# Kernel optimization log

Hardware: AMD Instinct MI355X
Metric: run time of the kernel (lower is better)

## Reference

```python
import jax, jax.numpy as jnp
import numpy as np

B, N, C = 4, 2048, 768
H = 12
HD = C // H
SCALE = HD ** -0.5


def setup_inputs() -> dict:
    key = jax.random.key(0)
    k1, k2, k3 = jax.random.split(key, 3)
    x = jax.random.normal(k1, (B, N, C), dtype=jnp.float32)
    w_qkv = jax.random.normal(k2, (3 * C, C), dtype=jnp.float32) * (C ** -0.5)
    w_proj = jax.random.normal(k3, (C, C), dtype=jnp.float32) * (C ** -0.5)
    b_proj = jnp.zeros((C,), dtype=jnp.float32)
    return {"x": x, "w_qkv": w_qkv, "w_proj": w_proj, "b_proj": b_proj}


def reference(x, w_qkv, w_proj, b_proj):
    Bx, Nx, Cx = x.shape
    # qkv linear: x @ W^T -> [B, N, 3C], then split into heads
    qkv = jnp.einsum('bnc,dc->bnd', x, w_qkv)
    qkv = qkv.reshape(Bx, Nx, 3, H, HD).transpose(2, 0, 3, 1, 4)  # [3, B, H, N, HD]
    q, k, v = qkv[0], qkv[1], qkv[2]
    attn = jnp.einsum('bhqd,bhkd->bhqk', q, k) * SCALE  # [B, H, N, N]
    attn = jax.nn.softmax(attn, axis=-1)
    out = jnp.einsum('bhqk,bhkd->bhqd', attn, v)  # [B, H, N, HD]
    out = out.transpose(0, 2, 1, 3).reshape(Bx, Nx, Cx)
    out = jnp.einsum('bnc,dc->bnd', out, w_proj) + b_proj
    return out
```

## Files before the change

kernel.cpp:

```cpp
#include <hip/hip_runtime.h>
#include <hip/hip_bf16.h>
#include <stdint.h>

#define DI __device__ __forceinline__

typedef __bf16 bf16x8 __attribute__((ext_vector_type(8)));
typedef float f32x4 __attribute__((ext_vector_type(4)));
typedef uint32_t u32x4 __attribute__((ext_vector_type(4)));
typedef unsigned short u16;

DI u16 f2bf(float f) {
  union { float f; uint32_t u; } x; x.f = f;
  uint32_t r = (x.u + 0x7FFFu + ((x.u >> 16) & 1u)) >> 16;
  return (u16)r;
}
DI bf16x8 load16(const u16* p) { return *(const bf16x8*)p; }

DI void async_copy16(void* lds, const void* g) {
  __builtin_amdgcn_global_load_lds(
      (const __attribute__((address_space(1))) uint32_t*)g,
      (__attribute__((address_space(3))) uint32_t*)lds, 16, 0, 0);
}

DI f32x4 mfma16(bf16x8 a, bf16x8 b, f32x4 c) {
  return __builtin_amdgcn_mfma_f32_16x16x32_bf16(a, b, c, 0, 0, 0);
}

DI uint32_t pk_bf16(float a, float b) {
  union { __hip_bfloat162 v; uint32_t u; } r;
  r.v = __float22bfloat162_rn(make_float2(a, b));
  return r.u;
}

DI void permlane32_swap(uint32_t &a, uint32_t &b) {
  asm("v_permlane32_swap_b32 %0, %1" : "+v"(a), "+v"(b));
}

#define QSCALE (0.125f * 1.44269504088896340736f)

__global__ __launch_bounds__(256)
void cvt_all(const float* __restrict__ s0, u16* __restrict__ d0, int n0,
             const float* __restrict__ s1, u16* __restrict__ d1, int n1,
             const float* __restrict__ s2, u16* __restrict__ d2, int n2) {
  int i = (blockIdx.x * 256 + threadIdx.x) * 4;
  const float* s; u16* d;
  if (i < n0) { s = s0 + i; d = d0 + i; }
  else if (i < n0 + n1) { s = s1 + (i - n0); d = d1 + (i - n0); }
  else if (i < n0 + n1 + n2) { s = s2 + (i - n0 - n1); d = d2 + (i - n0 - n1); }
  else return;
  float4 v = *(const float4*)s;
  ushort4 o;
  o.x = f2bf(v.x); o.y = f2bf(v.y); o.z = f2bf(v.z); o.w = f2bf(v.w);
  *(ushort4*)d = o;
}

__global__ __launch_bounds__(256)
void gemm_qkv(const u16* __restrict__ A, const u16* __restrict__ Bm,
              u16* __restrict__ Qb, u16* __restrict__ Kb, u16* __restrict__ Vt,
              int M, int N, int K) {
  __shared__ u16 As[128 * 32];
  __shared__ u16 Bs[128 * 32];

  const int tid  = threadIdx.x;
  const int lane = tid & 63;
  const int wave = tid >> 6;
  const int lb  = blockIdx.x + 18 * blockIdx.y;
  const int swz = (lb & 7) * 144 + (lb >> 3);
  const int n0 = (swz % 18) * 128;
  const int m0 = (swz / 18) * 128;
  const int wm = (wave & 1) * 64;
  const int wn = (wave >> 1) * 64;
  const int c = lane & 15;
  const int g = lane >> 4;

  f32x4 acc[4][4] = {};

  for (int k0 = 0; k0 < K; k0 += 32) {
#pragma unroll
    for (int i = 0; i < 2; ++i) {
      int j = i * 256 + tid;
      int row = j >> 2;
      int col = (j & 3) * 8;
      async_copy16(&As[j * 8], &A[(size_t)(m0 + row) * K + k0 + col]);
      async_copy16(&Bs[j * 8], &Bm[(size_t)(n0 + row) * K + k0 + col]);
    }
    __syncthreads();

    bf16x8 af[4], bfr[4];
#pragma unroll
    for (int t = 0; t < 4; ++t) {
      af[t]  = *(const bf16x8*)&As[(wm + t * 16 + c) * 32 + g * 8];
      bfr[t] = *(const bf16x8*)&Bs[(wn + t * 16 + c) * 32 + g * 8];
    }
#pragma unroll
    for (int mt = 0; mt < 4; ++mt)
#pragma unroll
      for (int nt = 0; nt < 4; ++nt)
        acc[mt][nt] = mfma16(af[mt], bfr[nt], acc[mt][nt]);
    __syncthreads();
  }

  if (n0 < 768) {
#pragma unroll
    for (int nt = 0; nt < 4; ++nt) {
      int col = n0 + wn + nt * 16 + c;
#pragma unroll
      for (int mt = 0; mt < 4; ++mt)
#pragma unroll
        for (int r = 0; r < 4; ++r) {
          int row = m0 + wm + mt * 16 + g * 4 + r;
          Qb[(size_t)row * 768 + col] = f2bf(acc[mt][nt][r] * QSCALE);
        }
    }
  } else if (n0 < 1536) {
#pragma unroll
    for (int nt = 0; nt < 4; ++nt) {
      int col = n0 - 768 + wn + nt * 16 + c;
#pragma unroll
      for (int mt = 0; mt < 4; ++mt)
#pragma unroll
        for (int r = 0; r < 4; ++r) {
          int row = m0 + wm + mt * 16 + g * 4 + r;
          Kb[(size_t)row * 768 + col] = f2bf(acc[mt][nt][r]);
        }
    }
  } else {
#pragma unroll
    for (int nt = 0; nt < 4; ++nt) {
      int cv = n0 - 1536 + wn + nt * 16 + c;
      int hv = cv >> 6, d = cv & 63;
#pragma unroll
      for (int mt = 0; mt < 4; ++mt) {
        int row = m0 + wm + mt * 16 + g * 4;
        int b = row >> 11, nn = row & 2047;
        ushort4 o;
        o.x = f2bf(acc[mt][nt][0]); o.y = f2bf(acc[mt][nt][1]);
        o.z = f2bf(acc[mt][nt][2]); o.w = f2bf(acc[mt][nt][3]);
        *(ushort4*)&Vt[(((size_t)b * 12 + hv) * 64 + d) * 2048 + nn] = o;
      }
    }
  }
}

__global__ __launch_bounds__(256)
void gemm_proj(const u16* __restrict__ A, const u16* __restrict__ Bm,
               const float* __restrict__ bias, float* __restrict__ Co,
               int M, int N, int K) {
  __shared__ u16 As[128 * 32];
  __shared__ u16 Bs[128 * 32];

  const int tid  = threadIdx.x;
  const int lane = tid & 63;
  const int wave = tid >> 6;
  const int lb  = blockIdx.x + 6 * blockIdx.y;
  const int swz = (lb & 7) * 48 + (lb >> 3);
  const int n0 = (swz % 6) * 128;
  const int m0 = (swz / 6) * 128;
  const int wm = (wave & 1) * 64;
  const int wn = (wave >> 1) * 64;
  const int c = lane & 15;
  const int g = lane >> 4;

  f32x4 acc[4][4] = {};

  for (int k0 = 0; k0 < K; k0 += 32) {
#pragma unroll
    for (int i = 0; i < 2; ++i) {
      int j = i * 256 + tid;
      int row = j >> 2;
      int col = (j & 3) * 8;
      async_copy16(&As[j * 8], &A[(size_t)(m0 + row) * K + k0 + col]);
      async_copy16(&Bs[j * 8], &Bm[(size_t)(n0 + row) * K + k0 + col]);
    }
    __syncthreads();

    bf16x8 af[4], bfr[4];
#pragma unroll
    for (int t = 0; t < 4; ++t) {
      af[t]  = *(const bf16x8*)&As[(wm + t * 16 + c) * 32 + g * 8];
      bfr[t] = *(const bf16x8*)&Bs[(wn + t * 16 + c) * 32 + g * 8];
    }
#pragma unroll
    for (int mt = 0; mt < 4; ++mt)
#pragma unroll
      for (int nt = 0; nt < 4; ++nt)
        acc[mt][nt] = mfma16(af[mt], bfr[nt], acc[mt][nt]);
    __syncthreads();
  }

#pragma unroll
  for (int nt = 0; nt < 4; ++nt) {
    int col = n0 + wn + nt * 16 + c;
    float bv = bias[col];
#pragma unroll
    for (int mt = 0; mt < 4; ++mt)
#pragma unroll
      for (int r = 0; r < 4; ++r) {
        int row = m0 + wm + mt * 16 + g * 4 + r;
        Co[(size_t)row * N + col] = acc[mt][nt][r] + bv;
      }
  }
}

__global__ __launch_bounds__(256)
void attn_flash(const u16* __restrict__ Qb, const u16* __restrict__ Kb,
                const u16* __restrict__ Vt, u16* __restrict__ out) {
  __shared__ u16 Ks[2][2 * 64 * 32];
  __shared__ u16 Vs[2][2 * 64 * 32];

  const int tid  = threadIdx.x;
  const int lane = tid & 63;
  const int wave = tid >> 6;
  const int bid = blockIdx.x;
  const int swz = (bid & 7) * 96 + (bid >> 3);
  const int qchunk = swz & 15;
  const int h = (swz >> 4) % 12;
  const int b = swz / 192;
  const int q0 = qchunk * 128 + wave * 32;
  const int c = lane & 15;
  const int g = lane >> 4;
  const int g_odd = g & 1;

  const u16* Qp = Qb + (size_t)b * 2048 * 768 + h * 64;
  const u16* Kp = Kb + (size_t)b * 2048 * 768 + h * 64;
  const u16* Vp = Vt + ((size_t)b * 12 + h) * 64 * 2048;

  const bf16x8 qf0 = load16(&Qp[(size_t)(q0 + c) * 768 + g * 8]);
  const bf16x8 qf1 = load16(&Qp[(size_t)(q0 + c) * 768 + 32 + g * 8]);
  const bf16x8 qg0 = load16(&Qp[(size_t)(q0 + 16 + c) * 768 + g * 8]);
  const bf16x8 qg1 = load16(&Qp[(size_t)(q0 + 16 + c) * 768 + 32 + g * 8]);

  const int kk = tid >> 2;
  const int ch = (tid & 3) * 8;

  float lsum0 = 0.f, lsum1 = 0.f;
  f32x4 o0[4] = {}, o1[4] = {};

  async_copy16(&Ks[0][tid * 8],        &Kp[(size_t)kk * 768 + ch]);
  async_copy16(&Ks[0][2048 + tid * 8], &Kp[(size_t)kk * 768 + 32 + ch]);
  async_copy16(&Vs[0][tid * 8],        &Vp[(size_t)kk * 2048 + ch]);
  async_copy16(&Vs[0][2048 + tid * 8], &Vp[(size_t)kk * 2048 + 32 + ch]);

  int cur = 0;
  for (int k0 = 0; k0 < 2048; k0 += 64) {
    __syncthreads();

    if (k0 + 64 < 2048) {
      int nxt = cur ^ 1, kn = k0 + 64;
      async_copy16(&Ks[nxt][tid * 8],        &Kp[(size_t)(kn + kk) * 768 + ch]);
      async_copy16(&Ks[nxt][2048 + tid * 8], &Kp[(size_t)(kn + kk) * 768 + 32 + ch]);
      async_copy16(&Vs[nxt][tid * 8],        &Vp[(size_t)kk * 2048 + kn + ch]);
      async_copy16(&Vs[nxt][2048 + tid * 8], &Vp[(size_t)kk * 2048 + kn + 32 + ch]);
    }

    f32x4 s0[4] = {}, s1[4] = {};
#pragma unroll
    for (int kt = 0; kt < 4; ++kt) {
      bf16x8 kf0 = *(const bf16x8*)&Ks[cur][(kt * 16 + c) * 32 + g * 8];
      bf16x8 kf1 = *(const bf16x8*)&Ks[cur][2048 + (kt * 16 + c) * 32 + g * 8];
      s0[kt] = mfma16(kf0, qf0, s0[kt]);
      s0[kt] = mfma16(kf1, qf1, s0[kt]);
      s1[kt] = mfma16(kf0, qg0, s1[kt]);
      s1[kt] = mfma16(kf1, qg1, s1[kt]);
    }

    bf16x8 PA0[2], PA1[2];
#pragma unroll
    for (int kt2 = 0; kt2 < 2; ++kt2) {
#pragma unroll
      for (int sub = 0; sub < 2; ++sub) {
        const f32x4 sa = sub ? s1[2 * kt2] : s0[2 * kt2];
        const f32x4 sb = sub ? s1[2 * kt2 + 1] : s0[2 * kt2 + 1];
        float e0 = __builtin_amdgcn_exp2f(sa[0]);
        float e1 = __builtin_amdgcn_exp2f(sa[1]);
        float e2 = __builtin_amdgcn_exp2f(sa[2]);
        float e3 = __builtin_amdgcn_exp2f(sa[3]);
        float f0 = __builtin_amdgcn_exp2f(sb[0]);
        float f1 = __builtin_amdgcn_exp2f(sb[1]);
        float f2 = __builtin_amdgcn_exp2f(sb[2]);
        float f3 = __builtin_amdgcn_exp2f(sb[3]);
        float sum = ((e0 + e1) + (e2 + e3)) + ((f0 + f1) + (f2 + f3));
        if (sub) lsum1 += sum; else lsum0 += sum;
        uint32_t E0 = pk_bf16(e0, e1);
        uint32_t E1 = pk_bf16(e2, e3);
        uint32_t F0 = pk_bf16(f0, f1);
        uint32_t F1 = pk_bf16(f2, f3);
        permlane32_swap(E0, F0);
        permlane32_swap(E1, F1);
        uint32_t Z0 = __shfl_xor(F0, 16);
        uint32_t Z1 = __shfl_xor(F1, 16);
        uint32_t Y0 = __shfl_xor(E0, 16);
        uint32_t Y1 = __shfl_xor(E1, 16);
        union { u32x4 u; bf16x8 v; } pa;
        pa.u.x = g_odd ? Z0 : E0;
        pa.u.y = g_odd ? Z1 : E1;
        pa.u.z = g_odd ? F0 : Y0;
        pa.u.w = g_odd ? F1 : Y1;
        if (sub) PA1[kt2] = pa.v; else PA0[kt2] = pa.v;
      }
    }

#pragma unroll
    for (int kt2 = 0; kt2 < 2; ++kt2) {
#pragma unroll
      for (int dt = 0; dt < 4; ++dt) {
        bf16x8 vf = *(const bf16x8*)&Vs[cur][kt2 * 2048 + (dt * 16 + c) * 32 + g * 8];
        o0[dt] = mfma16(PA0[kt2], vf, o0[dt]);
        o1[dt] = mfma16(PA1[kt2], vf, o1[dt]);
      }
    }
    cur ^= 1;
  }

  float t0 = lsum0 + __shfl_xor(lsum0, 16);
  t0 += __shfl_xor(t0, 32);
  float t1 = lsum1 + __shfl_xor(lsum1, 16);
  t1 += __shfl_xor(t1, 32);
  float inv0 = 1.f / t0;
  float inv1 = 1.f / t1;
  float invr0[4], invr1[4];
#pragma unroll
  for (int r = 0; r < 4; ++r) {
    invr0[r] = __shfl(inv0, g * 4 + r);
    invr1[r] = __shfl(inv1, g * 4 + r);
  }

#pragma unroll
  for (int dt = 0; dt < 4; ++dt)
#pragma unroll
    for (int r = 0; r < 4; ++r) {
      int n = q0 + g * 4 + r;
      out[(size_t)(b * 2048 + n) * 768 + h * 64 + dt * 16 + c] =
          f2bf(o0[dt][r] * invr0[r]);
      out[(size_t)(b * 2048 + n + 16) * 768 + h * 64 + dt * 16 + c] =
          f2bf(o1[dt][r] * invr1[r]);
    }
}

extern "C" void kernel_launch(void* const* d_in, const int* in_sizes, int n_in,
                              void* d_out, int out_size, void* d_ws, size_t ws_size,
                              hipStream_t stream) {
  const float* x      = (const float*)d_in[0];
  const float* w_qkv  = (const float*)d_in[1];
  const float* w_proj = (const float*)d_in[2];
  const float* b_proj = (const float*)d_in[3];
  float* out = (float*)d_out;

  const int M = 8192;
  const int C = 768;
  const int NQKV = 2304;

  u16* xb     = (u16*)d_ws;
  u16* wqkvb  = xb + (size_t)M * C;
  u16* wprojb = wqkvb + (size_t)NQKV * C;
  u16* Qb     = wprojb + (size_t)C * C;
  u16* Kb     = Qb + (size_t)M * C;
  u16* Vt     = Kb + (size_t)M * C;
  u16* attn   = Vt + (size_t)M * C;

  dim3 blk(256);
  const int n0 = M * C, n1 = NQKV * C, n2 = C * C;
  cvt_all<<<dim3((n0 + n1 + n2) / 1024), blk, 0, stream>>>(
      x, xb, n0, w_qkv, wqkvb, n1, w_proj, wprojb, n2);

  gemm_qkv<<<dim3(NQKV / 128, M / 128), blk, 0, stream>>>(
      xb, wqkvb, Qb, Kb, Vt, M, NQKV, C);
  attn_flash<<<dim3(4 * 12 * 16), blk, 0, stream>>>(Qb, Kb, Vt, attn);
  gemm_proj<<<dim3(C / 128, M / 128), blk, 0, stream>>>(
      attn, wprojb, b_proj, out, M, C, C);
}
```

Before: 229.5 us.

## Stage K/V through registers with XOR-swizzled LDS layout in flash attention

```diff
diff --git a/kernel.cpp b/kernel.cpp
--- a/kernel.cpp
+++ b/kernel.cpp
@@ -220,6 +220,7 @@
   const int c = lane & 15;
   const int g = lane >> 4;
   const int g_odd = g & 1;
+  const int sw = (g ^ (c & 3)) * 8;
 
   const u16* Qp = Qb + (size_t)b * 2048 * 768 + h * 64;
   const u16* Kp = Kb + (size_t)b * 2048 * 768 + h * 64;
@@ -230,34 +231,39 @@
   const bf16x8 qg0 = load16(&Qp[(size_t)(q0 + 16 + c) * 768 + g * 8]);
   const bf16x8 qg1 = load16(&Qp[(size_t)(q0 + 16 + c) * 768 + 32 + g * 8]);
 
-  const int kk = tid >> 2;
-  const int ch = (tid & 3) * 8;
+  const int kk  = tid >> 2;
+  const int chs = (((tid >> 2) & 3) ^ (tid & 3)) * 8;
 
   float lsum0 = 0.f, lsum1 = 0.f;
   f32x4 o0[4] = {}, o1[4] = {};
 
-  async_copy16(&Ks[0][tid * 8],        &Kp[(size_t)kk * 768 + ch]);
-  async_copy16(&Ks[0][2048 + tid * 8], &Kp[(size_t)kk * 768 + 32 + ch]);
-  async_copy16(&Vs[0][tid * 8],        &Vp[(size_t)kk * 2048 + ch]);
-  async_copy16(&Vs[0][2048 + tid * 8], &Vp[(size_t)kk * 2048 + 32 + ch]);
+  uint4 rk0 = *(const uint4*)&Kp[(size_t)kk * 768 + chs];
+  uint4 rk1 = *(const uint4*)&Kp[(size_t)kk * 768 + 32 + chs];
+  uint4 rv0 = *(const uint4*)&Vp[(size_t)kk * 2048 + chs];
+  uint4 rv1 = *(const uint4*)&Vp[(size_t)kk * 2048 + 32 + chs];
+  *(uint4*)&Ks[0][tid * 8]        = rk0;
+  *(uint4*)&Ks[0][2048 + tid * 8] = rk1;
+  *(uint4*)&Vs[0][tid * 8]        = rv0;
+  *(uint4*)&Vs[0][2048 + tid * 8] = rv1;
 
   int cur = 0;
   for (int k0 = 0; k0 < 2048; k0 += 64) {
     __syncthreads();
 
-    if (k0 + 64 < 2048) {
-      int nxt = cur ^ 1, kn = k0 + 64;
-      async_copy16(&Ks[nxt][tid * 8],        &Kp[(size_t)(kn + kk) * 768 + ch]);
-      async_copy16(&Ks[nxt][2048 + tid * 8], &Kp[(size_t)(kn + kk) * 768 + 32 + ch]);
-      async_copy16(&Vs[nxt][tid * 8],        &Vp[(size_t)kk * 2048 + kn + ch]);
-      async_copy16(&Vs[nxt][2048 + tid * 8], &Vp[(size_t)kk * 2048 + kn + 32 + ch]);
+    const bool pf = (k0 + 64 < 2048);
+    if (pf) {
+      int kn = k0 + 64;
+      rk0 = *(const uint4*)&Kp[(size_t)(kn + kk) * 768 + chs];
+      rk1 = *(const uint4*)&Kp[(size_t)(kn + kk) * 768 + 32 + chs];
+      rv0 = *(const uint4*)&Vp[(size_t)kk * 2048 + kn + chs];
+      rv1 = *(const uint4*)&Vp[(size_t)kk * 2048 + kn + 32 + chs];
     }
 
     f32x4 s0[4] = {}, s1[4] = {};
 #pragma unroll
     for (int kt = 0; kt < 4; ++kt) {
-      bf16x8 kf0 = *(const bf16x8*)&Ks[cur][(kt * 16 + c) * 32 + g * 8];
-      bf16x8 kf1 = *(const bf16x8*)&Ks[cur][2048 + (kt * 16 + c) * 32 + g * 8];
+      bf16x8 kf0 = *(const bf16x8*)&Ks[cur][(kt * 16 + c) * 32 + sw];
+      bf16x8 kf1 = *(const bf16x8*)&Ks[cur][2048 + (kt * 16 + c) * 32 + sw];
       s0[kt] = mfma16(kf0, qf0, s0[kt]);
       s0[kt] = mfma16(kf1, qf1, s0[kt]);
       s1[kt] = mfma16(kf0, qg0, s1[kt]);
@@ -304,10 +310,18 @@
     for (int kt2 = 0; kt2 < 2; ++kt2) {
 #pragma unroll
       for (int dt = 0; dt < 4; ++dt) {
-        bf16x8 vf = *(const bf16x8*)&Vs[cur][kt2 * 2048 + (dt * 16 + c) * 32 + g * 8];
+        bf16x8 vf = *(const bf16x8*)&Vs[cur][kt2 * 2048 + (dt * 16 + c) * 32 + sw];
         o0[dt] = mfma16(PA0[kt2], vf, o0[dt]);
         o1[dt] = mfma16(PA1[kt2], vf, o1[dt]);
       }
+    }
+
+    if (pf) {
+      int nxt = cur ^ 1;
+      *(uint4*)&Ks[nxt][tid * 8]        = rk0;
+      *(uint4*)&Ks[nxt][2048 + tid * 8] = rk1;
+      *(uint4*)&Vs[nxt][tid * 8]        = rv0;
+      *(uint4*)&Vs[nxt][2048 + tid * 8] = rv1;
     }
     cur ^= 1;
   }
```

Result: slower. 237.6 us (+3.5%).

## Permute V tile layout at load time to drop cross-lane P shuffles

Applied to the files above, without the earlier changes.

```diff
diff --git a/kernel.cpp b/kernel.cpp
--- a/kernel.cpp
+++ b/kernel.cpp
@@ -30,10 +30,6 @@
   union { __hip_bfloat162 v; uint32_t u; } r;
   r.v = __float22bfloat162_rn(make_float2(a, b));
   return r.u;
-}
-
-DI void permlane32_swap(uint32_t &a, uint32_t &b) {
-  asm("v_permlane32_swap_b32 %0, %1" : "+v"(a), "+v"(b));
 }
 
 #define QSCALE (0.125f * 1.44269504088896340736f)
@@ -219,7 +215,6 @@
   const int q0 = qchunk * 128 + wave * 32;
   const int c = lane & 15;
   const int g = lane >> 4;
-  const int g_odd = g & 1;
 
   const u16* Qp = Qb + (size_t)b * 2048 * 768 + h * 64;
   const u16* Kp = Kb + (size_t)b * 2048 * 768 + h * 64;
@@ -232,25 +227,39 @@
 
   const int kk = tid >> 2;
   const int ch = (tid & 3) * 8;
+  const int vq = tid & 3;
+  const size_t vrow = (size_t)kk * 2048;
 
   float lsum0 = 0.f, lsum1 = 0.f;
   f32x4 o0[4] = {}, o1[4] = {};
 
   async_copy16(&Ks[0][tid * 8],        &Kp[(size_t)kk * 768 + ch]);
   async_copy16(&Ks[0][2048 + tid * 8], &Kp[(size_t)kk * 768 + 32 + ch]);
-  async_copy16(&Vs[0][tid * 8],        &Vp[(size_t)kk * 2048 + ch]);
-  async_copy16(&Vs[0][2048 + tid * 8], &Vp[(size_t)kk * 2048 + 32 + ch]);
+  {
+    uint2 a0 = *(const uint2*)&Vp[vrow + 4 * vq];
+    uint2 a1 = *(const uint2*)&Vp[vrow + 16 + 4 * vq];
+    uint2 b0 = *(const uint2*)&Vp[vrow + 32 + 4 * vq];
+    uint2 b1 = *(const uint2*)&Vp[vrow + 48 + 4 * vq];
+    uint4 w0; w0.x = a0.x; w0.y = a0.y; w0.z = a1.x; w0.w = a1.y;
+    uint4 w1; w1.x = b0.x; w1.y = b0.y; w1.z = b1.x; w1.w = b1.y;
+    *(uint4*)&Vs[0][tid * 8]        = w0;
+    *(uint4*)&Vs[0][2048 + tid * 8] = w1;
+  }
 
   int cur = 0;
   for (int k0 = 0; k0 < 2048; k0 += 64) {
     __syncthreads();
 
-    if (k0 + 64 < 2048) {
+    const bool pf = (k0 + 64 < 2048);
+    uint2 a0, a1, b0, b1;
+    if (pf) {
       int nxt = cur ^ 1, kn = k0 + 64;
       async_copy16(&Ks[nxt][tid * 8],        &Kp[(size_t)(kn + kk) * 768 + ch]);
       async_copy16(&Ks[nxt][2048 + tid * 8], &Kp[(size_t)(kn + kk) * 768 + 32 + ch]);
-      async_copy16(&Vs[nxt][tid * 8],        &Vp[(size_t)kk * 2048 + kn + ch]);
-      async_copy16(&Vs[nxt][2048 + tid * 8], &Vp[(size_t)kk * 2048 + kn + 32 + ch]);
+      a0 = *(const uint2*)&Vp[vrow + kn + 4 * vq];
+      a1 = *(const uint2*)&Vp[vrow + kn + 16 + 4 * vq];
+      b0 = *(const uint2*)&Vp[vrow + kn + 32 + 4 * vq];
+      b1 = *(const uint2*)&Vp[vrow + kn + 48 + 4 * vq];
     }
 
     f32x4 s0[4] = {}, s1[4] = {};
@@ -267,10 +276,8 @@
     bf16x8 PA0[2], PA1[2];
 #pragma unroll
     for (int kt2 = 0; kt2 < 2; ++kt2) {
-#pragma unroll
-      for (int sub = 0; sub < 2; ++sub) {
-        const f32x4 sa = sub ? s1[2 * kt2] : s0[2 * kt2];
-        const f32x4 sb = sub ? s1[2 * kt2 + 1] : s0[2 * kt2 + 1];
+      {
+        const f32x4 sa = s0[2 * kt2], sb = s0[2 * kt2 + 1];
         float e0 = __builtin_amdgcn_exp2f(sa[0]);
         float e1 = __builtin_amdgcn_exp2f(sa[1]);
         float e2 = __builtin_amdgcn_exp2f(sa[2]);
@@ -279,24 +286,31 @@
         float f1 = __builtin_amdgcn_exp2f(sb[1]);
         float f2 = __builtin_amdgcn_exp2f(sb[2]);
         float f3 = __builtin_amdgcn_exp2f(sb[3]);
-        float sum = ((e0 + e1) + (e2 + e3)) + ((f0 + f1) + (f2 + f3));
-        if (sub) lsum1 += sum; else lsum0 += sum;
-        uint32_t E0 = pk_bf16(e0, e1);
-        uint32_t E1 = pk_bf16(e2, e3);
-        uint32_t F0 = pk_bf16(f0, f1);
-        uint32_t F1 = pk_bf16(f2, f3);
-        permlane32_swap(E0, F0);
-        permlane32_swap(E1, F1);
-        uint32_t Z0 = __shfl_xor(F0, 16);
-        uint32_t Z1 = __shfl_xor(F1, 16);
-        uint32_t Y0 = __shfl_xor(E0, 16);
-        uint32_t Y1 = __shfl_xor(E1, 16);
+        lsum0 += ((e0 + e1) + (e2 + e3)) + ((f0 + f1) + (f2 + f3));
         union { u32x4 u; bf16x8 v; } pa;
-        pa.u.x = g_odd ? Z0 : E0;
-        pa.u.y = g_odd ? Z1 : E1;
-        pa.u.z = g_odd ? F0 : Y0;
-        pa.u.w = g_odd ? F1 : Y1;
-        if (sub) PA1[kt2] = pa.v; else PA0[kt2] = pa.v;
+        pa.u.x = pk_bf16(e0, e1);
+        pa.u.y = pk_bf16(e2, e3);
+        pa.u.z = pk_bf16(f0, f1);
+        pa.u.w = pk_bf16(f2, f3);
+        PA0[kt2] = pa.v;
+      }
+      {
+        const f32x4 sa = s1[2 * kt2], sb = s1[2 * kt2 + 1];
+        float e0 = __builtin_amdgcn_exp2f(sa[0]);
+        float e1 = __builtin_amdgcn_exp2f(sa[1]);
+        float e2 = __builtin_amdgcn_exp2f(sa[2]);
+        float e3 = __builtin_amdgcn_exp2f(sa[3]);
+        float f0 = __builtin_amdgcn_exp2f(sb[0]);
+        float f1 = __builtin_amdgcn_exp2f(sb[1]);
+        float f2 = __builtin_amdgcn_exp2f(sb[2]);
+        float f3 = __builtin_amdgcn_exp2f(sb[3]);
+        lsum1 += ((e0 + e1) + (e2 + e3)) + ((f0 + f1) + (f2 + f3));
+        union { u32x4 u; bf16x8 v; } pa;
+        pa.u.x = pk_bf16(e0, e1);
+        pa.u.y = pk_bf16(e2, e3);
+        pa.u.z = pk_bf16(f0, f1);
+        pa.u.w = pk_bf16(f2, f3);
+        PA1[kt2] = pa.v;
       }
     }
 
@@ -308,6 +322,14 @@
         o0[dt] = mfma16(PA0[kt2], vf, o0[dt]);
         o1[dt] = mfma16(PA1[kt2], vf, o1[dt]);
       }
+    }
+
+    if (pf) {
+      int nxt = cur ^ 1;
+      uint4 w0; w0.x = a0.x; w0.y = a0.y; w0.z = a1.x; w0.w = a1.y;
+      uint4 w1; w1.x = b0.x; w1.y = b0.y; w1.z = b1.x; w1.w = b1.y;
+      *(uint4*)&Vs[nxt][tid * 8]        = w0;
+      *(uint4*)&Vs[nxt][2048 + tid * 8] = w1;
     }
     cur ^= 1;
   }
```

New measurement: 245.9 us. +7.2%, slower.

## Use 8 waves per attention block with one 16-row Q tile each and permuted V staging

Applied to the files above, without the earlier changes.

```diff
diff --git a/kernel.cpp b/kernel.cpp
--- a/kernel.cpp
+++ b/kernel.cpp
@@ -30,10 +30,6 @@
   union { __hip_bfloat162 v; uint32_t u; } r;
   r.v = __float22bfloat162_rn(make_float2(a, b));
   return r.u;
-}
-
-DI void permlane32_swap(uint32_t &a, uint32_t &b) {
-  asm("v_permlane32_swap_b32 %0, %1" : "+v"(a), "+v"(b));
 }
 
 #define QSCALE (0.125f * 1.44269504088896340736f)
@@ -202,11 +198,11 @@
   }
 }
 
-__global__ __launch_bounds__(256)
+__global__ __launch_bounds__(512)
 void attn_flash(const u16* __restrict__ Qb, const u16* __restrict__ Kb,
                 const u16* __restrict__ Vt, u16* __restrict__ out) {
-  __shared__ u16 Ks[2][2 * 64 * 32];
-  __shared__ u16 Vs[2][2 * 64 * 32];
+  __shared__ u16 Ks[2][64 * 64];
+  __shared__ u16 Vs[2][64 * 64];
 
   const int tid  = threadIdx.x;
   const int lane = tid & 63;
@@ -216,10 +212,9 @@
   const int qchunk = swz & 15;
   const int h = (swz >> 4) % 12;
   const int b = swz / 192;
-  const int q0 = qchunk * 128 + wave * 32;
+  const int q0 = qchunk * 128 + wave * 16;
   const int c = lane & 15;
   const int g = lane >> 4;
-  const int g_odd = g & 1;
 
   const u16* Qp = Qb + (size_t)b * 2048 * 768 + h * 64;
   const u16* Kp = Kb + (size_t)b * 2048 * 768 + h * 64;
@@ -227,103 +222,94 @@
 
   const bf16x8 qf0 = load16(&Qp[(size_t)(q0 + c) * 768 + g * 8]);
   const bf16x8 qf1 = load16(&Qp[(size_t)(q0 + c) * 768 + 32 + g * 8]);
-  const bf16x8 qg0 = load16(&Qp[(size_t)(q0 + 16 + c) * 768 + g * 8]);
-  const bf16x8 qg1 = load16(&Qp[(size_t)(q0 + 16 + c) * 768 + 32 + g * 8]);
-
-  const int kk = tid >> 2;
-  const int ch = (tid & 3) * 8;
-
-  float lsum0 = 0.f, lsum1 = 0.f;
-  f32x4 o0[4] = {}, o1[4] = {};
-
-  async_copy16(&Ks[0][tid * 8],        &Kp[(size_t)kk * 768 + ch]);
-  async_copy16(&Ks[0][2048 + tid * 8], &Kp[(size_t)kk * 768 + 32 + ch]);
-  async_copy16(&Vs[0][tid * 8],        &Vp[(size_t)kk * 2048 + ch]);
-  async_copy16(&Vs[0][2048 + tid * 8], &Vp[(size_t)kk * 2048 + 32 + ch]);
+
+  const int krow = tid >> 3;
+  const int khalf = (tid >> 2) & 1;
+  const int kchq = tid & 3;
+  const size_t kgoff = (size_t)krow * 768 + khalf * 32 + kchq * 8;
+  const int vrow = tid >> 3;
+  const int vkt2 = (tid >> 2) & 1;
+  const int vgq = tid & 3;
+  const size_t vbase = (size_t)vrow * 2048 + vkt2 * 32 + 4 * vgq;
+
+  float lsum = 0.f;
+  f32x4 o0[4] = {};
+
+  async_copy16(&Ks[0][tid * 8], &Kp[kgoff]);
+  {
+    uint2 a0 = *(const uint2*)&Vp[vbase];
+    uint2 a1 = *(const uint2*)&Vp[vbase + 16];
+    uint4 w; w.x = a0.x; w.y = a0.y; w.z = a1.x; w.w = a1.y;
+    *(uint4*)&Vs[0][tid * 8] = w;
+  }
 
   int cur = 0;
   for (int k0 = 0; k0 < 2048; k0 += 64) {
     __syncthreads();
 
-    if (k0 + 64 < 2048) {
-      int nxt = cur ^ 1, kn = k0 + 64;
-      async_copy16(&Ks[nxt][tid * 8],        &Kp[(size_t)(kn + kk) * 768 + ch]);
-      async_copy16(&Ks[nxt][2048 + tid * 8], &Kp[(size_t)(kn + kk) * 768 + 32 + ch]);
-      async_copy16(&Vs[nxt][tid * 8],        &Vp[(size_t)kk * 2048 + kn + ch]);
-      async_copy16(&Vs[nxt][2048 + tid * 8], &Vp[(size_t)kk * 2048 + kn + 32 + ch]);
-    }
-
-    f32x4 s0[4] = {}, s1[4] = {};
+    const bool pf = (k0 + 64 < 2048);
+    uint2 a0, a1;
+    if (pf) {
+      int nxt = cur ^ 1;
+      async_copy16(&Ks[nxt][tid * 8], &Kp[(size_t)(k0 + 64) * 768 + kgoff]);
+      a0 = *(const uint2*)&Vp[vbase + k0 + 64];
+      a1 = *(const uint2*)&Vp[vbase + k0 + 64 + 16];
+    }
+
+    f32x4 s0[4] = {};
 #pragma unroll
     for (int kt = 0; kt < 4; ++kt) {
-      bf16x8 kf0 = *(const bf16x8*)&Ks[cur][(kt * 16 + c) * 32 + g * 8];
-      bf16x8 kf1 = *(const bf16x8*)&Ks[cur][2048 + (kt * 16 + c) * 32 + g * 8];
+      bf16x8 kf0 = *(const bf16x8*)&Ks[cur][(kt * 16 + c) * 64 + g * 8];
+      bf16x8 kf1 = *(const bf16x8*)&Ks[cur][(kt * 16 + c) * 64 + 32 + g * 8];
       s0[kt] = mfma16(kf0, qf0, s0[kt]);
       s0[kt] = mfma16(kf1, qf1, s0[kt]);
-      s1[kt] = mfma16(kf0, qg0, s1[kt]);
-      s1[kt] = mfma16(kf1, qg1, s1[kt]);
-    }
-
-    bf16x8 PA0[2], PA1[2];
+    }
+
+    bf16x8 PA[2];
 #pragma unroll
     for (int kt2 = 0; kt2 < 2; ++kt2) {
-#pragma unroll
-      for (int sub = 0; sub < 2; ++sub) {
-        const f32x4 sa = sub ? s1[2 * kt2] : s0[2 * kt2];
-        const f32x4 sb = sub ? s1[2 * kt2 + 1] : s0[2 * kt2 + 1];
-        float e0 = __builtin_amdgcn_exp2f(sa[0]);
-        float e1 = __builtin_amdgcn_exp2f(sa[1]);
-        float e2 = __builtin_amdgcn_exp2f(sa[2]);
-        float e3 = __builtin_amdgcn_exp2f(sa[3]);
-        float f0 = __builtin_amdgcn_exp2f(sb[0]);
-        float f1 = __builtin_amdgcn_exp2f(sb[1]);
-        float f2 = __builtin_amdgcn_exp2f(sb[2]);
-        float f3 = __builtin_amdgcn_exp2f(sb[3]);
-        float sum = ((e0 + e1) + (e2 + e3)) + ((f0 + f1) + (f2 + f3));
-        if (sub) lsum1 += sum; else lsum0 += sum;
-        uint32_t E0 = pk_bf16(e0, e1);
-        uint32_t E1 = pk_bf16(e2, e3);
-        uint32_t F0 = pk_bf16(f0, f1);
-        uint32_t F1 = pk_bf16(f2, f3);
-        permlane32_swap(E0, F0);
-        permlane32_swap(E1, F1);
-        uint32_t Z0 = __shfl_xor(F0, 16);
-        uint32_t Z1 = __shfl_xor(F1, 16);
-        uint32_t Y0 = __shfl_xor(E0, 16);
-        uint32_t Y1 = __shfl_xor(E1, 16);
-        union { u32x4 u; bf16x8 v; } pa;
-        pa.u.x = g_odd ? Z0 : E0;
-        pa.u.y = g_odd ? Z1 : E1;
-        pa.u.z = g_odd ? F0 : Y0;
-        pa.u.w = g_odd ? F1 : Y1;
-        if (sub) PA1[kt2] = pa.v; else PA0[kt2] = pa.v;
+      const f32x4 sa = s0[2 * kt2], sb = s0[2 * kt2 + 1];
+      float e0 = __builtin_amdgcn_exp2f(sa[0]);
+      float e1 = __builtin_amdgcn_exp2f(sa[1]);
+      float e2 = __builtin_amdgcn_exp2f(sa[2]);
+      float e3 = __builtin_amdgcn_exp2f(sa[3]);
+      float f0 = __builtin_amdgcn_exp2f(sb[0]);
+      float f1 = __builtin_amdgcn_exp2f(sb[1]);
+      float f2 = __builtin_amdgcn_exp2f(sb[2]);
+      float f3 = __builtin_amdgcn_exp2f(sb[3]);
+      lsum += ((e0 + e1) + (e2 + e3)) + ((f0 + f1) + (f2 + f3));
+      union { u32x4 u; bf16x8 v; } pa;
+      pa.u.x = pk_bf16(e0, e1);
+      pa.u.y = pk_bf16(e2, e3);
+      pa.u.z = pk_bf16(f0, f1);
+      pa.u.w = pk_bf16(f2, f3);
+      PA[kt2] = pa.v;
+    }
+
+#pragma unroll
+    for (int kt2 = 0; kt2 < 2; ++kt2) {
+#pragma unroll
+      for (int dt = 0; dt < 4; ++dt) {
+        bf16x8 vf = *(const bf16x8*)&Vs[cur][(dt * 16 + c) * 64 + kt2 * 32 + g * 8];
+        o0[dt] = mfma16(PA[kt2], vf, o0[dt]);
       }
     }
 
-#pragma unroll
-    for (int kt2 = 0; kt2 < 2; ++kt2) {
-#pragma unroll
-      for (int dt = 0; dt < 4; ++dt) {
-        bf16x8 vf = *(const bf16x8*)&Vs[cur][kt2 * 2048 + (dt * 16 + c) * 32 + g * 8];
-        o0[dt] = mfma16(PA0[kt2], vf, o0[dt]);
-        o1[dt] = mfma16(PA1[kt2], vf, o1[dt]);
-      }
+    if (pf) {
+      int nxt = cur ^ 1;
+      uint4 w; w.x = a0.x; w.y = a0.y; w.z = a1.x; w.w = a1.y;
+      *(uint4*)&Vs[nxt][tid * 8] = w;
     }
     cur ^= 1;
   }
 
-  float t0 = lsum0 + __shfl_xor(lsum0, 16);
+  float t0 = lsum + __shfl_xor(lsum, 16);
   t0 += __shfl_xor(t0, 32);
-  float t1 = lsum1 + __shfl_xor(lsum1, 16);
-  t1 += __shfl_xor(t1, 32);
   float inv0 = 1.f / t0;
-  float inv1 = 1.f / t1;
-  float invr0[4], invr1[4];
-#pragma unroll
-  for (int r = 0; r < 4; ++r) {
+  float invr0[4];
+#pragma unroll
+  for (int r = 0; r < 4; ++r)
     invr0[r] = __shfl(inv0, g * 4 + r);
-    invr1[r] = __shfl(inv1, g * 4 + r);
-  }
 
 #pragma unroll
   for (int dt = 0; dt < 4; ++dt)
@@ -332,8 +318,6 @@
       int n = q0 + g * 4 + r;
       out[(size_t)(b * 2048 + n) * 768 + h * 64 + dt * 16 + c] =
           f2bf(o0[dt][r] * invr0[r]);
-      out[(size_t)(b * 2048 + n + 16) * 768 + h * 64 + dt * 16 + c] =
-          f2bf(o1[dt][r] * invr1[r]);
     }
 }
 
@@ -365,7 +349,7 @@
 
   gemm_qkv<<<dim3(NQKV / 128, M / 128), blk, 0, stream>>>(
       xb, wqkvb, Qb, Kb, Vt, M, NQKV, C);
-  attn_flash<<<dim3(4 * 12 * 16), blk, 0, stream>>>(Qb, Kb, Vt, attn);
+  attn_flash<<<dim3(4 * 12 * 16), dim3(512), 0, stream>>>(Qb, Kb, Vt, attn);
   gemm_proj<<<dim3(C / 128, M / 128), blk, 0, stream>>>(
       attn, wprojb, b_proj, out, M, C, C);
 }
```

Result: slower. 254.5 us (+10.9%).
